# Kernel optimization log

Hardware: AMD Instinct MI355X
Metric: run time of the kernel (lower is better)

The kernel has to match this reference:

```python
import jax, jax.numpy as jnp
import numpy as np
from jax.scipy.linalg import expm

NUM_WIRES = 10
DIM = 2 ** NUM_WIRES  # 1024, statevector dimension
N_GATES = 8


def setup_inputs() -> dict:
    key = jax.random.key(0)
    kf, kg, kt = jax.random.split(key, 3)
    # feature to be amplitude-embedded (AmplitudeEmbedding pads with 0 and L2-normalizes)
    feature = jax.random.normal(kf, (DIM,), jnp.float32)
    # dense Hermitian gate generators (real symmetric), one per selected gate
    A = jax.random.normal(kg, (N_GATES, DIM, DIM), jnp.float32) / np.float32(np.sqrt(DIM))
    gens = 0.5 * (A + jnp.swapaxes(A, -1, -2))
    # learned parameters theta, shape (n_gates, 1) as in the flax module
    theta = jax.random.normal(kt, (N_GATES, 1), jnp.float32)
    return {"feature": feature, "theta": theta, "gens": gens}


def reference(feature, theta, gens):
    # AmplitudeEmbedding: pad (no-op here, len == DIM) then L2-normalize -> complex state
    psi = (feature / jnp.linalg.norm(feature)).astype(jnp.complex64)  # [DIM]

    def apply_gate(psi, gate):
        G, t = gate  # G: [DIM, DIM] complex, t: scalar complex
        U = expm(-1j * t * G)          # qml.exp(-1j * theta * gen)
        return U @ psi, None

    gens_c = gens.astype(jnp.complex64)
    thetas_c = theta[:, 0].astype(jnp.complex64)
    psi, _ = jax.lax.scan(apply_gate, psi, (gens_c, thetas_c))
    # qml.probs(wires=all): Born-rule probabilities over the full register
    return jnp.real(psi * jnp.conj(psi)).astype(jnp.float32)  # [DIM]
```

## Files before the change

kernel.cpp:

```cpp
#include <hip/hip_runtime.h>

#define DIM   1024
#define NG    8
#define NBLK  256
#define TPB   256
#define WAVES (TPB / 64)
#define SCALE    1.45f
#define INVSCALE (1.0f / SCALE)
#define CTOL  5e-3f
#define KMAX  12
#define SEGW  (2 * WAVES)

typedef unsigned long long u64;


__device__ __forceinline__ u64 packw(float v, unsigned seq) {
  union { float f; unsigned u; } c; c.f = v;
  return ((u64)seq << 32) | (u64)c.u;
}
__device__ __forceinline__ float unpackf(u64 x) {
  union { unsigned u; float f; } c; c.u = (unsigned)x;
  return c.f;
}

__global__ __launch_bounds__(TPB) void qsim_kernel(
    const float* __restrict__ feat,
    const float* __restrict__ theta,
    const float* __restrict__ gens,
    float*       __restrict__ out,
    u64*         __restrict__ vbuf0,
    u64*         __restrict__ vbuf1)
{
  const int tid  = threadIdx.x;
  const int lane = tid & 63;
  const int wid  = tid >> 6;
  const int bid  = blockIdx.x;
  const int row  = bid * WAVES + wid;

  __shared__ float2   smemV[DIM];
  __shared__ float2   smemPub[WAVES];
  __shared__ float    red[WAVES];
  __shared__ unsigned wdone;
  __shared__ unsigned ready;
  float* smemVf   = (float*)smemV;
  float* smemPubF = (float*)smemPub;

  float a[16];
  {
    const float* Gr = gens + (size_t)row * DIM;
    #pragma unroll
    for (int p = 0; p < 16; ++p) a[p] = Gr[p * 64 + lane];
  }

  if (tid == 0) { wdone = 0; ready = 0; }
  {
    float f0 = feat[tid],           f1 = feat[tid + TPB];
    float f2 = feat[tid + 2 * TPB], f3 = feat[tid + 3 * TPB];
    float s = f0 * f0 + f1 * f1 + f2 * f2 + f3 * f3;
    #pragma unroll
    for (int mm = 1; mm < 64; mm <<= 1) s += __shfl_xor(s, mm);
    if (lane == 0) red[wid] = s;
  }
  __syncthreads();
  float tot = 0.f;
  #pragma unroll
  for (int i = 0; i < WAVES; ++i) tot += red[i];
  const float inv = 1.0f / sqrtf(tot);

  float pr = feat[row] * inv;
  float pi = 0.f;

  unsigned pub = 0;
  bool  pend_anext = false;
  int   gnext = 0;
  float anext[16];

  auto publish = [&](float sr, float si) {
    if (lane == 0) smemPub[wid] = make_float2(sr, si);
    asm volatile("s_waitcnt lgkmcnt(0)" ::: "memory");
    unsigned old = 0;
    if (lane == 0) old = atomicAdd(&wdone, 1u);
    old = __shfl(old, 0);
    const unsigned seq = pub + 1;
    if (old == WAVES * seq - 1) {
      u64* dst = (seq & 1) ? vbuf1 : vbuf0;
      if (lane < SEGW) {
        const float f = smemPubF[lane];
        __hip_atomic_store(dst + bid * SEGW + lane, packw(f, seq),
                           __ATOMIC_RELAXED, __HIP_MEMORY_SCOPE_AGENT);
      }
    }
    ++pub;
  };

  auto issue_anext = [&]() {
    const float* Gr = gens + (size_t)gnext * DIM * DIM + (size_t)row * DIM;
    #pragma unroll
    for (int p = 0; p < 16; ++p) anext[p] = Gr[p * 64 + lane];
    pend_anext = false;
  };

  for (int g = 0; g < NG; ++g) {
    const float  th = theta[g];
    const double z  = (double)th * (double)SCALE;
    const double az = fmax(fabs(z), 1e-6);
    const float  sg = (th < 0.f) ? -1.f : 1.f;

    double bv[19];
    bv[18] = 1e-30;
    bv[17] = (36.0 / az) * 1e-30;
    #pragma unroll
    for (int k = 17; k >= 1; --k)
      bv[k - 1] = (2.0 * (double)k / az) * bv[k] - bv[k + 1];
    double S = bv[0];
    #pragma unroll
    for (int k = 2; k <= 18; k += 2) S += 2.0 * bv[k];
    const double invS = 1.0 / S;

    float jc[KMAX + 2];
    #pragma unroll
    for (int k = 0; k <= KMAX + 1; ++k) jc[k] = (float)(bv[k] * invS);

    int m = KMAX; bool found = false;
    #pragma unroll
    for (int k = 1; k <= KMAX; ++k) {
      if (!found && (double)(k + 1) > az &&
          fabs(bv[k + 1] * invS) < (double)CTOL) { m = k; found = true; }
    }

    float accr = jc[0] * pr, acci = jc[0] * pi;
    float wm1r = pr, wm1i = pi, wm2r = 0.f, wm2i = 0.f;

    #pragma unroll
    for (int k = 1; k <= KMAX; ++k) {
      if (k > m) break;

      float2 v[16];
      if (g == 0 && k == 1) {
        #pragma unroll
        for (int p = 0; p < 16; ++p)
          v[p] = make_float2(feat[p * 64 + lane] * inv, 0.f);
      } else {
        if (wid == 0) {
          const u64* vsrc = (pub & 1) ? vbuf1 : vbuf0;
          for (;;) {
            u64 x[32];
            #pragma unroll
            for (int c = 0; c < 32; ++c)
              x[c] = __hip_atomic_load(vsrc + c * 64 + lane,
                                       __ATOMIC_RELAXED, __HIP_MEMORY_SCOPE_AGENT);
            bool ok = true;
            #pragma unroll
            for (int c = 0; c < 32; ++c)
              ok = ok && ((unsigned)(x[c] >> 32) == pub);
            if (__all(ok)) {
              #pragma unroll
              for (int c = 0; c < 32; ++c) smemVf[c * 64 + lane] = unpackf(x[c]);
              break;
            }
            __builtin_amdgcn_s_sleep(2);
          }
          __hip_atomic_store(&ready, pub, __ATOMIC_RELEASE,
                             __HIP_MEMORY_SCOPE_WORKGROUP);
          if (pend_anext) issue_anext();
          #pragma unroll
          for (int p = 0; p < 16; ++p) v[p] = smemV[p * 64 + lane];
        } else {
          while ((int)(__hip_atomic_load(&ready, __ATOMIC_ACQUIRE,
                                         __HIP_MEMORY_SCOPE_WORKGROUP) - pub) < 0) {
            __builtin_amdgcn_s_sleep(1);
          }
          #pragma unroll
          for (int p = 0; p < 16; ++p) v[p] = smemV[p * 64 + lane];
        }
      }

      float yr = 0.f, yi = 0.f;
      #pragma unroll
      for (int p = 0; p < 16; ++p) {
        yr = fmaf(a[p], v[p].x, yr);
        yi = fmaf(a[p], v[p].y, yi);
      }
      #pragma unroll
      for (int mm = 1; mm < 64; mm <<= 1) {
        yr += __shfl_xor(yr, mm);
        yi += __shfl_xor(yi, mm);
      }

      const float ur = yr * INVSCALE;
      const float ui = yi * INVSCALE;
      const float wkr = (k == 1) ? ur : fmaf(2.f, ur, -wm2r);
      const float wki = (k == 1) ? ui : fmaf(2.f, ui, -wm2i);

      const bool last = (k == m);
      if (!last) publish(wkr, wki);

      {
        const float j2  = 2.f * jc[k];
        const float sj2 = sg * j2;
        if ((k & 3) == 0) {
          accr = fmaf(j2, wkr, accr);
          acci = fmaf(j2, wki, acci);
        } else if ((k & 3) == 1) {
          accr = fmaf( sj2, wki, accr);
          acci = fmaf(-sj2, wkr, acci);
        } else if ((k & 3) == 2) {
          accr = fmaf(-j2, wkr, accr);
          acci = fmaf(-j2, wki, acci);
        } else {
          accr = fmaf(-sj2, wki, accr);
          acci = fmaf( sj2, wkr, acci);
        }
      }

      if (k == 1 && g < NG - 1) {
        if (wid != 0) {
          const float* Gr = gens + (size_t)(g + 1) * DIM * DIM
                                 + (size_t)row * DIM;
          #pragma unroll
          for (int p = 0; p < 16; ++p) anext[p] = Gr[p * 64 + lane];
        } else {
          pend_anext = true; gnext = g + 1;
        }
      }

      if (last) {
        if (g < NG - 1) publish(accr, acci);
      } else {
        wm2r = wm1r; wm2i = wm1i;
        wm1r = wkr;  wm1i = wki;
      }
    }

    if (g < NG - 1) {
      if (wid == 0 && pend_anext) issue_anext();
      #pragma unroll
      for (int p = 0; p < 16; ++p) a[p] = anext[p];
    }
    pr = accr; pi = acci;
  }

  if (lane == 0) out[row] = pr * pr + pi * pi;
}

extern "C" void kernel_launch(void* const* d_in, const int* in_sizes, int n_in,
                              void* d_out, int out_size, void* d_ws, size_t ws_size,
                              hipStream_t stream) {
  const float* feat  = (const float*)d_in[0];
  const float* theta = (const float*)d_in[1];
  const float* gens  = (const float*)d_in[2];
  float* out = (float*)d_out;

  u64* vbuf0 = (u64*)d_ws;
  u64* vbuf1 = (u64*)((char*)d_ws + (size_t)DIM * 2 * sizeof(u64));

  qsim_kernel<<<dim3(NBLK), dim3(TPB), 0, stream>>>(
      feat, theta, gens, out, vbuf0, vbuf1);
}
```

Measured before the change: 140.9 us.

## Publish per-wave results directly and poll only pending chunks in grid sync

New measurement: 167.7 us. 1.19x slower.

```diff
diff --git a/kernel.cpp b/kernel.cpp
--- a/kernel.cpp
+++ b/kernel.cpp
@@ -9,7 +9,6 @@
 #define INVSCALE (1.0f / SCALE)
 #define CTOL  5e-3f
 #define KMAX  12
-#define SEGW  (2 * WAVES)
 
 typedef unsigned long long u64;
 
@@ -38,12 +37,9 @@
   const int row  = bid * WAVES + wid;
 
   __shared__ float2   smemV[DIM];
-  __shared__ float2   smemPub[WAVES];
   __shared__ float    red[WAVES];
-  __shared__ unsigned wdone;
   __shared__ unsigned ready;
-  float* smemVf   = (float*)smemV;
-  float* smemPubF = (float*)smemPub;
+  float* smemVf = (float*)smemV;
 
   float a[16];
   {
@@ -52,7 +48,7 @@
     for (int p = 0; p < 16; ++p) a[p] = Gr[p * 64 + lane];
   }
 
-  if (tid == 0) { wdone = 0; ready = 0; }
+  if (tid == 0) { ready = 0; }
   {
     float f0 = feat[tid],           f1 = feat[tid + TPB];
     float f2 = feat[tid + 2 * TPB], f3 = feat[tid + 3 * TPB];
@@ -76,19 +72,12 @@
   float anext[16];
 
   auto publish = [&](float sr, float si) {
-    if (lane == 0) smemPub[wid] = make_float2(sr, si);
-    asm volatile("s_waitcnt lgkmcnt(0)" ::: "memory");
-    unsigned old = 0;
-    if (lane == 0) old = atomicAdd(&wdone, 1u);
-    old = __shfl(old, 0);
     const unsigned seq = pub + 1;
-    if (old == WAVES * seq - 1) {
-      u64* dst = (seq & 1) ? vbuf1 : vbuf0;
-      if (lane < SEGW) {
-        const float f = smemPubF[lane];
-        __hip_atomic_store(dst + bid * SEGW + lane, packw(f, seq),
-                           __ATOMIC_RELAXED, __HIP_MEMORY_SCOPE_AGENT);
-      }
+    u64* dst = (seq & 1) ? vbuf1 : vbuf0;
+    if (lane < 2) {
+      const float f = (lane == 0) ? sr : si;
+      __hip_atomic_store(dst + (size_t)row * 2 + lane, packw(f, seq),
+                         __ATOMIC_RELAXED, __HIP_MEMORY_SCOPE_AGENT);
     }
     ++pub;
   };
@@ -143,23 +132,27 @@
       } else {
         if (wid == 0) {
           const u64* vsrc = (pub & 1) ? vbuf1 : vbuf0;
+          u64 x[32];
+          unsigned pend = 0xFFFFFFFFu;
           for (;;) {
-            u64 x[32];
             #pragma unroll
-            for (int c = 0; c < 32; ++c)
-              x[c] = __hip_atomic_load(vsrc + c * 64 + lane,
-                                       __ATOMIC_RELAXED, __HIP_MEMORY_SCOPE_AGENT);
-            bool ok = true;
+            for (int c = 0; c < 32; ++c) {
+              if (pend & (1u << c))
+                x[c] = __hip_atomic_load(vsrc + c * 64 + lane,
+                                         __ATOMIC_RELAXED, __HIP_MEMORY_SCOPE_AGENT);
+            }
+            unsigned np = 0;
             #pragma unroll
-            for (int c = 0; c < 32; ++c)
-              ok = ok && ((unsigned)(x[c] >> 32) == pub);
-            if (__all(ok)) {
-              #pragma unroll
-              for (int c = 0; c < 32; ++c) smemVf[c * 64 + lane] = unpackf(x[c]);
-              break;
+            for (int c = 0; c < 32; ++c) {
+              if ((pend & (1u << c)) && (unsigned)(x[c] >> 32) != pub)
+                np |= (1u << c);
             }
-            __builtin_amdgcn_s_sleep(2);
+            pend = np;
+            if (__all(pend == 0)) break;
+            __builtin_amdgcn_s_sleep(1);
           }
+          #pragma unroll
+          for (int c = 0; c < 32; ++c) smemVf[c * 64 + lane] = unpackf(x[c]);
           __hip_atomic_store(&ready, pub, __ATOMIC_RELEASE,
                              __HIP_MEMORY_SCOPE_WORKGROUP);
           if (pend_anext) issue_anext();
@@ -168,7 +161,6 @@
         } else {
           while ((int)(__hip_atomic_load(&ready, __ATOMIC_ACQUIRE,
                                          __HIP_MEMORY_SCOPE_WORKGROUP) - pub) < 0) {
-            __builtin_amdgcn_s_sleep(1);
           }
           #pragma unroll
           for (int p = 0; p < 16; ++p) v[p] = smemV[p * 64 + lane];
```

## Split global vector polling across all waves with counter-based intra-block barrier

Applied to the files above, without the earlier changes.

After: 129.5 us, median of 2. -8.1%, faster.

```diff
diff --git a/kernel.cpp b/kernel.cpp
--- a/kernel.cpp
+++ b/kernel.cpp
@@ -41,7 +41,7 @@
   __shared__ float2   smemPub[WAVES];
   __shared__ float    red[WAVES];
   __shared__ unsigned wdone;
-  __shared__ unsigned ready;
+  __shared__ unsigned rdy;
   float* smemVf   = (float*)smemV;
   float* smemPubF = (float*)smemPub;
 
@@ -52,7 +52,7 @@
     for (int p = 0; p < 16; ++p) a[p] = Gr[p * 64 + lane];
   }
 
-  if (tid == 0) { wdone = 0; ready = 0; }
+  if (tid == 0) { wdone = 0; rdy = 0; }
   {
     float f0 = feat[tid],           f1 = feat[tid + TPB];
     float f2 = feat[tid + 2 * TPB], f3 = feat[tid + 3 * TPB];
@@ -71,8 +71,7 @@
   float pi = 0.f;
 
   unsigned pub = 0;
-  bool  pend_anext = false;
-  int   gnext = 0;
+  unsigned nc  = 0;
   float anext[16];
 
   auto publish = [&](float sr, float si) {
@@ -93,13 +92,6 @@
     ++pub;
   };
 
-  auto issue_anext = [&]() {
-    const float* Gr = gens + (size_t)gnext * DIM * DIM + (size_t)row * DIM;
-    #pragma unroll
-    for (int p = 0; p < 16; ++p) anext[p] = Gr[p * 64 + lane];
-    pend_anext = false;
-  };
-
   for (int g = 0; g < NG; ++g) {
     const float  th = theta[g];
     const double z  = (double)th * (double)SCALE;
@@ -141,38 +133,47 @@
         for (int p = 0; p < 16; ++p)
           v[p] = make_float2(feat[p * 64 + lane] * inv, 0.f);
       } else {
-        if (wid == 0) {
-          const u64* vsrc = (pub & 1) ? vbuf1 : vbuf0;
-          for (;;) {
-            u64 x[32];
-            #pragma unroll
-            for (int c = 0; c < 32; ++c)
-              x[c] = __hip_atomic_load(vsrc + c * 64 + lane,
-                                       __ATOMIC_RELAXED, __HIP_MEMORY_SCOPE_AGENT);
-            bool ok = true;
-            #pragma unroll
-            for (int c = 0; c < 32; ++c)
-              ok = ok && ((unsigned)(x[c] >> 32) == pub);
-            if (__all(ok)) {
-              #pragma unroll
-              for (int c = 0; c < 32; ++c) smemVf[c * 64 + lane] = unpackf(x[c]);
-              break;
-            }
-            __builtin_amdgcn_s_sleep(2);
-          }
-          __hip_atomic_store(&ready, pub, __ATOMIC_RELEASE,
-                             __HIP_MEMORY_SCOPE_WORKGROUP);
-          if (pend_anext) issue_anext();
+        const u64* vsrc = (pub & 1) ? vbuf1 : vbuf0;
+        const int  qb   = wid * 512;
+        u64 x[8];
+        for (;;) {
           #pragma unroll
-          for (int p = 0; p < 16; ++p) v[p] = smemV[p * 64 + lane];
-        } else {
-          while ((int)(__hip_atomic_load(&ready, __ATOMIC_ACQUIRE,
-                                         __HIP_MEMORY_SCOPE_WORKGROUP) - pub) < 0) {
-            __builtin_amdgcn_s_sleep(1);
-          }
+          for (int c = 0; c < 8; ++c)
+            x[c] = __hip_atomic_load(vsrc + qb + c * 64 + lane,
+                                     __ATOMIC_RELAXED, __HIP_MEMORY_SCOPE_AGENT);
+          bool ok = true;
           #pragma unroll
-          for (int p = 0; p < 16; ++p) v[p] = smemV[p * 64 + lane];
-        }
+          for (int c = 0; c < 8; ++c)
+            ok = ok && ((unsigned)(x[c] >> 32) == pub);
+          if (__all(ok)) break;
+          __builtin_amdgcn_s_sleep(1);
+        }
+        #pragma unroll
+        for (int c = 0; c < 8; ++c)
+          smemVf[qb + c * 64 + lane] = unpackf(x[c]);
+        asm volatile("s_waitcnt lgkmcnt(0)" ::: "memory");
+        if (lane == 0)
+          __hip_atomic_fetch_add(&rdy, 1u, __ATOMIC_RELEASE,
+                                 __HIP_MEMORY_SCOPE_WORKGROUP);
+        if (k == 1 && g < NG - 1) {
+          const float* Gr = gens + (size_t)(g + 1) * DIM * DIM
+                                 + (size_t)row * DIM;
+          #pragma unroll
+          for (int p = 0; p < 16; ++p) anext[p] = Gr[p * 64 + lane];
+        }
+        ++nc;
+        while ((int)(__hip_atomic_load(&rdy, __ATOMIC_ACQUIRE,
+                                       __HIP_MEMORY_SCOPE_WORKGROUP)
+                     - WAVES * nc) < 0) {
+        }
+        #pragma unroll
+        for (int p = 0; p < 16; ++p) v[p] = smemV[p * 64 + lane];
+      }
+
+      if (g == 0 && k == 1) {
+        const float* Gr = gens + (size_t)DIM * DIM + (size_t)row * DIM;
+        #pragma unroll
+        for (int p = 0; p < 16; ++p) anext[p] = Gr[p * 64 + lane];
       }
 
       float yr = 0.f, yi = 0.f;
@@ -213,17 +214,6 @@
         }
       }
 
-      if (k == 1 && g < NG - 1) {
-        if (wid != 0) {
-          const float* Gr = gens + (size_t)(g + 1) * DIM * DIM
-                                 + (size_t)row * DIM;
-          #pragma unroll
-          for (int p = 0; p < 16; ++p) anext[p] = Gr[p * 64 + lane];
-        } else {
-          pend_anext = true; gnext = g + 1;
-        }
-      }
-
       if (last) {
         if (g < NG - 1) publish(accr, acci);
       } else {
@@ -233,7 +223,6 @@
     }
 
     if (g < NG - 1) {
-      if (wid == 0 && pend_anext) issue_anext();
       #pragma unroll
       for (int p = 0; p < 16; ++p) a[p] = anext[p];
     }
```
